# Optimization experiments

Measured on AMD Instinct MI355X. Metric: run time of the kernel, lower is better.

Reference implementation:

```python
import jax, jax.numpy as jnp
import numpy as np
import math

H = 16  # n_heads


def setup_inputs() -> dict:
    key = jax.random.key(0)
    ks = jax.random.split(key, 12)
    B, S, D = 8, 1024, 1024
    inp = {
        "query": jax.random.normal(ks[0], (B, S, D), jnp.float32),
        "key_": jax.random.normal(ks[1], (B, S, D), jnp.float32),
        "value": jax.random.normal(ks[2], (B, S, D), jnp.float32),
        "mask": jnp.ones((B, S, S), jnp.int32),
        "attn_pos": jax.random.normal(ks[3], (1, H, S, S), jnp.float32),
    }
    sc = 1.0 / math.sqrt(D)
    for i, nm in enumerate(["q", "k", "v", "o"]):
        inp[f"w{nm}"] = jax.random.normal(ks[4 + i], (D, D), jnp.float32) * sc
        inp[f"b{nm}"] = jax.random.normal(ks[8 + i], (D,), jnp.float32) * 0.01
    return inp


def reference(query, key_, value, mask, attn_pos, wq, bq, wk, bk, wv, bv, wo, bo):
    B, S, D = query.shape
    dk = D // H

    def proj(x, w, b):  # [B,S,D] -> [B,H,S,dk]
        return (x @ w.T + b).reshape(B, S, H, dk).transpose(0, 2, 1, 3)

    q = proj(query, wq, bq)
    k = proj(key_, wk, bk)
    v = proj(value, wv, bv)

    # attn_pos branch: scale by sqrt(2*d_k), add positional bias
    scores = jnp.einsum("bhqd,bhkd->bhqk", q, k) / math.sqrt(2 * dk) + attn_pos
    scores = jnp.where(mask[:, None] == 0, -1e9, scores)
    p = jax.nn.softmax(scores, axis=-1)  # dropout inactive (eval)
    x = jnp.einsum("bhqk,bhkd->bhqd", p, v)
    x = x.transpose(0, 2, 1, 3).reshape(B, S, D)
    x = x @ wo.T + bo          # linears[-1] applied once...
    return x @ wo.T + bo       # ...and again, faithful to source
```

## Files before the change

kernel.cpp:

```cpp
#include <hip/hip_runtime.h>
#include <hip/hip_bf16.h>

typedef unsigned short u16;
typedef unsigned int u32;
typedef __attribute__((ext_vector_type(8))) short bfrag;
typedef __attribute__((ext_vector_type(4))) float f32x4;

#define DEVINL __device__ __forceinline__

DEVINL u16 f2bf(float f) {
  u32 u = __float_as_uint(f);
  u32 r = (u + 0x7fffu + ((u >> 16) & 1u)) >> 16;
  return (u16)r;
}
DEVINL float bf2f(u16 u) { return __uint_as_float(((u32)u) << 16); }
DEVINL u32 cvtpk(float lo, float hi) {
  u32 r;
  asm("v_cvt_pk_bf16_f32 %0, %1, %2" : "=v"(r) : "v"(lo), "v"(hi));
  return r;
}
DEVINL u16 f2bf_hw(float v) { return (u16)cvtpk(v, v); }
DEVINL float fmax3(float a, float b, float c) { return fmaxf(fmaxf(a, b), c); }

DEVINL void gload_lds16(const void* g, void* l) {
  __builtin_amdgcn_global_load_lds(
      (const __attribute__((address_space(1))) void*)g,
      (__attribute__((address_space(3))) void*)l, 16, 0, 0);
}

DEVINL void storeC(u16* C, size_t idx, float v) { C[idx] = f2bf_hw(v); }
DEVINL void storeC(float* C, size_t idx, float v) { C[idx] = v; }


__global__ void cast_v4(const float* __restrict__ in, u16* __restrict__ out, int n4, float s) {
  const int i = blockIdx.x * 256 + threadIdx.x;
  if (i < n4) {
    const float4 f = ((const float4*)in)[i];
    uint2 r;
    r.x = cvtpk(f.x * s, f.y * s);
    r.y = cvtpk(f.z * s, f.w * s);
    ((uint2*)out)[i] = r;
  }
}

__global__ void pack_mask(const int* __restrict__ mask, u32* __restrict__ bits) {
  const size_t wi = (size_t)blockIdx.x * 256 + threadIdx.x;
  const int* src = mask + wi * 32;
  u32 v = 0;
#pragma unroll
  for (int i = 0; i < 8; ++i) {
    const int4 m4 = ((const int4*)src)[i];
    if (m4.x) v |= 1u << (i * 4 + 0);
    if (m4.y) v |= 1u << (i * 4 + 1);
    if (m4.z) v |= 1u << (i * 4 + 2);
    if (m4.w) v |= 1u << (i * 4 + 3);
  }
  bits[wi] = v;
}

__global__ void transpose_cast(const float* __restrict__ in, u16* __restrict__ out) {
  __shared__ u16 tile[64][65];
  const int t = threadIdx.x;
  const int bx = blockIdx.x, by = blockIdx.y;
#pragma unroll
  for (int p = 0; p < 4; ++p) {
    const int r = (t >> 4) + p * 16;
    const int c = (t & 15) * 4;
    const float4 f = *(const float4*)&in[(size_t)(by * 64 + r) * 1024 + bx * 64 + c];
    tile[c + 0][r] = f2bf(f.x);
    tile[c + 1][r] = f2bf(f.y);
    tile[c + 2][r] = f2bf(f.z);
    tile[c + 3][r] = f2bf(f.w);
  }
  __syncthreads();
#pragma unroll
  for (int p = 0; p < 4; ++p) {
    const int r = (t >> 4) + p * 16;
    const int c = (t & 15) * 4;
    uint2 v;
    v.x = (u32)tile[r][c] | ((u32)tile[r][c + 1] << 16);
    v.y = (u32)tile[r][c + 2] | ((u32)tile[r][c + 3] << 16);
    *(uint2*)&out[(size_t)(bx * 64 + r) * 1024 + by * 64 + c] = v;
  }
}

__global__ void bias2(const float* __restrict__ wo, const float* __restrict__ bo,
                      float* __restrict__ bo2) {
  const int w = threadIdx.x >> 6, lane = threadIdx.x & 63;
  const int row = blockIdx.x * 4 + w;
  const float* src = wo + (size_t)row * 1024;
  float s = 0.f;
#pragma unroll
  for (int i = 0; i < 4; ++i) {
    const float4 f = *(const float4*)&src[lane * 4 + i * 256];
    const float4 g = *(const float4*)&bo[lane * 4 + i * 256];
    s += f.x * g.x + f.y * g.y + f.z * g.z + f.w * g.w;
  }
#pragma unroll
  for (int d = 1; d < 64; d <<= 1) s += __shfl_xor(s, d);
  if (lane == 0) bo2[row] = s + bo[row];
}

__global__ __launch_bounds__(256) void gemm_bt_64(
    const u16* __restrict__ A, const u16* __restrict__ W,
    u16* __restrict__ C, int N, int K) {
  __shared__ u16 sA[64 * 64];
  __shared__ u16 sB[64 * 64];
  const int t = threadIdx.x;
  const int w = t >> 6, lane = t & 63;
  const int lr = lane & 15, lk = (lane >> 4) * 8;
  const int m0 = blockIdx.x * 64, n0 = blockIdx.y * 64;
  f32x4 acc[4] = {};
  for (int k0 = 0; k0 < K; k0 += 64) {
#pragma unroll
    for (int i = 0; i < 2; ++i) {
      const int idx = i * 256 + t;
      const int row = idx >> 3;
      const int col = (idx & 7) * 8;
      gload_lds16(A + (size_t)(m0 + row) * K + k0 + col, &sA[idx * 8]);
      gload_lds16(W + (size_t)(n0 + row) * K + k0 + col, &sB[idx * 8]);
    }
    __syncthreads();
#pragma unroll
    for (int ks = 0; ks < 2; ++ks) {
      const bfrag av = *(const bfrag*)&sA[(w * 16 + lr) * 64 + ks * 32 + lk];
#pragma unroll
      for (int n = 0; n < 4; ++n) {
        const bfrag bv = *(const bfrag*)&sB[(n * 16 + lr) * 64 + ks * 32 + lk];
        acc[n] = __builtin_amdgcn_mfma_f32_16x16x32_bf16(av, bv, acc[n], 0, 0, 0);
      }
    }
    __syncthreads();
  }
  const int orow = (lane >> 4) * 4;
#pragma unroll
  for (int n = 0; n < 4; ++n)
#pragma unroll
    for (int j = 0; j < 4; ++j)
      C[(size_t)(m0 + w * 16 + orow + j) * N + n0 + n * 16 + lr] = f2bf_hw(acc[n][j]);
}


template <typename OutT>
__global__ __launch_bounds__(256) void gemm_bt_a16(
    const u16* __restrict__ A, const u16* __restrict__ W,
    const float* __restrict__ bias, OutT* __restrict__ C,
    int M, int N, int K) {
  __shared__ __align__(16) u16 sA[128 * 64];
  __shared__ __align__(16) u16 sB[128 * 64];
  const int t = threadIdx.x;
  const int w = t >> 6, lane = t & 63;
  const int lr = lane & 15, lg = lane >> 4;
  const int m0 = blockIdx.x * 128, n0 = blockIdx.y * 128;
  const int wr = (w >> 1) * 64, wc = (w & 1) * 64;
  f32x4 acc[4][4] = {};

  for (int k0 = 0; k0 < K; k0 += 64) {
#pragma unroll
    for (int i = 0; i < 4; ++i) {
      const int idx = i * 256 + t;
      const int row = idx >> 3;
      const int col = ((idx & 7) ^ (row & 7)) * 8;
      gload_lds16(A + (size_t)(m0 + row) * K + k0 + col, (char*)sA + idx * 16);
      gload_lds16(W + (size_t)(n0 + row) * K + k0 + col, (char*)sB + idx * 16);
    }
    __syncthreads();
#pragma unroll
    for (int ks = 0; ks < 2; ++ks) {
      bfrag av[4], bv[4];
#pragma unroll
      for (int m = 0; m < 4; ++m) {
        const int row = wr + m * 16 + lr;
        av[m] = *(const bfrag*)((const char*)sA + row * 128 + ((ks * 64 + lg * 16) ^ ((row & 7) << 4)));
      }
#pragma unroll
      for (int n = 0; n < 4; ++n) {
        const int row = wc + n * 16 + lr;
        bv[n] = *(const bfrag*)((const char*)sB + row * 128 + ((ks * 64 + lg * 16) ^ ((row & 7) << 4)));
      }
#pragma unroll
      for (int m = 0; m < 4; ++m)
#pragma unroll
        for (int n = 0; n < 4; ++n)
          acc[m][n] = __builtin_amdgcn_mfma_f32_16x16x32_bf16(av[m], bv[n], acc[m][n], 0, 0, 0);
    }
    __syncthreads();
  }

  float bz[4];
#pragma unroll
  for (int n = 0; n < 4; ++n) bz[n] = bias[n0 + wc + n * 16 + lr];
  const int orow = lg * 4;
#pragma unroll
  for (int m = 0; m < 4; ++m) {
#pragma unroll
    for (int n = 0; n < 4; ++n) {
      const int r = m0 + wr + m * 16 + orow;
      const int c = n0 + wc + n * 16 + lr;
#pragma unroll
      for (int j = 0; j < 4; ++j)
        storeC(C, (size_t)(r + j) * N + c, acc[m][n][j] + bz[n]);
    }
  }
}

template <typename OutT>
__global__ __launch_bounds__(256) void gemm_bt_a32(
    const float* __restrict__ A, const u16* __restrict__ W,
    const float* __restrict__ bias, OutT* __restrict__ C,
    int M, int N, int K, float oscale) {
  __shared__ __align__(16) u16 sA[128 * 64];
  __shared__ __align__(16) u16 sB[128 * 64];
  const int t = threadIdx.x;
  const int w = t >> 6, lane = t & 63;
  const int lr = lane & 15, lg = lane >> 4;
  const int m0 = blockIdx.x * 128, n0 = blockIdx.y * 128;
  const int wr = (w >> 1) * 64, wc = (w & 1) * 64;
  f32x4 acc[4][4] = {};

  for (int k0 = 0; k0 < K; k0 += 64) {
#pragma unroll
    for (int i = 0; i < 4; ++i) {
      const int idx = i * 256 + t;
      const int row = idx >> 3;
      const int cg = idx & 7;
      const float* src = A + (size_t)(m0 + row) * K + k0 + cg * 8;
      const float4 f0 = *(const float4*)src;
      const float4 f1 = *(const float4*)(src + 4);
      uint4 pk;
      pk.x = cvtpk(f0.x, f0.y);
      pk.y = cvtpk(f0.z, f0.w);
      pk.z = cvtpk(f1.x, f1.y);
      pk.w = cvtpk(f1.z, f1.w);
      *(uint4*)((char*)sA + row * 128 + ((cg ^ (row & 7)) * 16)) = pk;
      gload_lds16(W + (size_t)(n0 + row) * K + k0 + ((cg ^ (row & 7)) * 8), (char*)sB + idx * 16);
    }
    __syncthreads();
#pragma unroll
    for (int ks = 0; ks < 2; ++ks) {
      bfrag av[4], bv[4];
#pragma unroll
      for (int m = 0; m < 4; ++m) {
        const int row = wr + m * 16 + lr;
        av[m] = *(const bfrag*)((const char*)sA + row * 128 + ((ks * 64 + lg * 16) ^ ((row & 7) << 4)));
      }
#pragma unroll
      for (int n = 0; n < 4; ++n) {
        const int row = wc + n * 16 + lr;
        bv[n] = *(const bfrag*)((const char*)sB + row * 128 + ((ks * 64 + lg * 16) ^ ((row & 7) << 4)));
      }
#pragma unroll
      for (int m = 0; m < 4; ++m)
#pragma unroll
        for (int n = 0; n < 4; ++n)
          acc[m][n] = __builtin_amdgcn_mfma_f32_16x16x32_bf16(av[m], bv[n], acc[m][n], 0, 0, 0);
    }
    __syncthreads();
  }

  float bz[4];
#pragma unroll
  for (int n = 0; n < 4; ++n) bz[n] = bias[n0 + wc + n * 16 + lr];
  const int orow = lg * 4;
#pragma unroll
  for (int m = 0; m < 4; ++m) {
#pragma unroll
    for (int n = 0; n < 4; ++n) {
      const int r = m0 + wr + m * 16 + orow;
      const int c = n0 + wc + n * 16 + lr;
#pragma unroll
      for (int j = 0; j < 4; ++j)
        storeC(C, (size_t)(r + j) * N + c, (acc[m][n][j] + bz[n]) * oscale);
    }
  }
}

__global__ __launch_bounds__(256) void gemm_bt_a32_vt(
    const float* __restrict__ A, const u16* __restrict__ W,
    const float* __restrict__ bias, u16* __restrict__ Vt,
    int M, int N, int K) {
  __shared__ __align__(16) u16 sA[128 * 64];
  __shared__ __align__(16) u16 sB[128 * 64];
  const int t = threadIdx.x;
  const int w = t >> 6, lane = t & 63;
  const int lr = lane & 15, lg = lane >> 4;
  const int m0 = blockIdx.x * 128, n0 = blockIdx.y * 128;
  const int wr = (w >> 1) * 64, wc = (w & 1) * 64;
  f32x4 acc[4][4] = {};

  for (int k0 = 0; k0 < K; k0 += 64) {
#pragma unroll
    for (int i = 0; i < 4; ++i) {
      const int idx = i * 256 + t;
      const int row = idx >> 3;
      const int cg = idx & 7;
      const float* src = A + (size_t)(m0 + row) * K + k0 + cg * 8;
      const float4 f0 = *(const float4*)src;
      const float4 f1 = *(const float4*)(src + 4);
      uint4 pk;
      pk.x = cvtpk(f0.x, f0.y);
      pk.y = cvtpk(f0.z, f0.w);
      pk.z = cvtpk(f1.x, f1.y);
      pk.w = cvtpk(f1.z, f1.w);
      *(uint4*)((char*)sA + row * 128 + ((cg ^ (row & 7)) * 16)) = pk;
      gload_lds16(W + (size_t)(n0 + row) * K + k0 + ((cg ^ (row & 7)) * 8), (char*)sB + idx * 16);
    }
    __syncthreads();
#pragma unroll
    for (int ks = 0; ks < 2; ++ks) {
      bfrag av[4], bv[4];
#pragma unroll
      for (int m = 0; m < 4; ++m) {
        const int row = wr + m * 16 + lr;
        av[m] = *(const bfrag*)((const char*)sA + row * 128 + ((ks * 64 + lg * 16) ^ ((row & 7) << 4)));
      }
#pragma unroll
      for (int n = 0; n < 4; ++n) {
        const int row = wc + n * 16 + lr;
        bv[n] = *(const bfrag*)((const char*)sB + row * 128 + ((ks * 64 + lg * 16) ^ ((row & 7) << 4)));
      }
#pragma unroll
      for (int m = 0; m < 4; ++m)
#pragma unroll
        for (int n = 0; n < 4; ++n)
          acc[m][n] = __builtin_amdgcn_mfma_f32_16x16x32_bf16(av[m], bv[n], acc[m][n], 0, 0, 0);
    }
    __syncthreads();
  }

  float bz[4];
#pragma unroll
  for (int n = 0; n < 4; ++n) bz[n] = bias[n0 + wc + n * 16 + lr];
  const int orow = lg * 4;
#pragma unroll
  for (int m = 0; m < 4; ++m) {
#pragma unroll
    for (int n = 0; n < 4; ++n) {
      const int r0 = m0 + wr + m * 16 + orow;
      const int c = n0 + wc + n * 16 + lr;
      const int bb = r0 >> 10, s = r0 & 1023;
      const int h = c >> 6, d = c & 63;
      uint2 v;
      v.x = cvtpk(acc[m][n][0] + bz[n], acc[m][n][1] + bz[n]);
      v.y = cvtpk(acc[m][n][2] + bz[n], acc[m][n][3] + bz[n]);
      *(uint2*)&Vt[(((size_t)bb * 16 + h) * 64 + d) * 1024 + s] = v;
    }
  }
}


__global__ __launch_bounds__(512, 4) void attn_fwd(
    const u16* __restrict__ Qm, const u16* __restrict__ Km,
    const u16* __restrict__ Vt, const float* __restrict__ pos,
    const u32* __restrict__ mbits, u16* __restrict__ Om) {
  const int bb = blockIdx.x >> 3;
  const int qt = blockIdx.x & 7;
  const int h = blockIdx.y;
  const int t = threadIdx.x;
  const int w = t >> 6, lane = t & 63;
  const int lr = lane & 15, lg = lane >> 4;
  const float log2e = 1.4426950408889634f;

  __shared__ __align__(16) char smem[49152];

  const int q0 = qt * 128;
  const size_t baseQ = ((size_t)bb * 1024) * 1024 + (size_t)h * 64;
  const size_t baseV = ((size_t)(bb * 16 + h) * 64) * 1024;
  const int qg = q0 + w * 16 + lr;
  const float* posrow = pos + ((size_t)h * 1024 + qg) * 1024;
  const u32* mrow = mbits + ((size_t)bb * 1024 + qg) * 32;

#pragma unroll
  for (int i = 0; i < 2; ++i) {
    const int idx = i * 512 + t;
    const int r = idx >> 3;
    const int w8 = idx & 7;
    gload_lds16(Qm + baseQ + (size_t)(q0 + r) * 1024 + (w8 ^ (r & 7)) * 8, smem + idx * 16);
  }
  {
    const int r = t >> 3;
    const int w8 = t & 7;
    gload_lds16(Km + baseQ + (size_t)r * 1024 + (w8 ^ (r & 7)) * 8, smem + 16384 + t * 16);
    gload_lds16(Vt + baseV + (size_t)r * 1024 + (w8 ^ (r & 7)) * 8, smem + 24576 + t * 16);
  }

  u32 ok = 0xffffffffu;
#pragma unroll
  for (int i = 0; i < 8; ++i) {
    const uint4 m4 = *(const uint4*)&mrow[i * 4];
    ok &= m4.x & m4.y & m4.z & m4.w;
  }
  const bool allone = __all(ok == 0xffffffffu);

  float4 pz[4];
#pragma unroll
  for (int n = 0; n < 4; ++n) pz[n] = *(const float4*)&posrow[n * 16 + lg * 4];

  __syncthreads();

  bfrag qv[2];
#pragma unroll
  for (int ks = 0; ks < 2; ++ks) {
    const int byt = (w * 16 + lr) * 128 + ((ks * 64 + lg * 16) ^ ((lr & 7) << 4));
    qv[ks] = *(const bfrag*)(smem + byt);
  }
  __syncthreads();

  f32x4 o[4] = {};
  float m_q = -3.0e38f, l_q = 0.f;

  for (int kt = 0; kt < 16; ++kt) {
    const int cur = kt & 1;
    const char* sK = smem + (cur ? 0 : 16384);
    const char* sV = smem + (cur ? 8192 : 24576);

    float4 pzn[4];
    if (kt < 15) {
      const int kn = (kt + 1) * 64;
      char* dK = smem + (cur ? 16384 : 0);
      char* dV = smem + (cur ? 24576 : 8192);
      const int r = t >> 3;
      const int w8 = t & 7;
      gload_lds16(Km + baseQ + (size_t)(kn + r) * 1024 + (w8 ^ (r & 7)) * 8, dK + t * 16);
      gload_lds16(Vt + baseV + (size_t)r * 1024 + kn + (w8 ^ (r & 7)) * 8, dV + t * 16);
#pragma unroll
      for (int n = 0; n < 4; ++n) pzn[n] = *(const float4*)&posrow[kn + n * 16 + lg * 4];
    }

    f32x4 s[4] = {};
    __builtin_amdgcn_s_setprio(1);
#pragma unroll
    for (int ks = 0; ks < 2; ++ks) {
#pragma unroll
      for (int n = 0; n < 4; ++n) {
        const int byt = (n * 16 + lr) * 128 + ((ks * 64 + lg * 16) ^ ((lr & 7) << 4));
        const bfrag kf = *(const bfrag*)(sK + byt);
        s[n] = __builtin_amdgcn_mfma_f32_16x16x32_bf16(kf, qv[ks], s[n], 0, 0, 0);
      }
    }
    __builtin_amdgcn_s_setprio(0);

    float pv[16];
#pragma unroll
    for (int n = 0; n < 4; ++n) {
      pv[n * 4 + 0] = fmaf(pz[n].x, log2e, s[n][0]);
      pv[n * 4 + 1] = fmaf(pz[n].y, log2e, s[n][1]);
      pv[n * 4 + 2] = fmaf(pz[n].z, log2e, s[n][2]);
      pv[n * 4 + 3] = fmaf(pz[n].w, log2e, s[n][3]);
    }

    if (!allone) {
      const u32 a0 = mrow[kt * 2], a1 = mrow[kt * 2 + 1];
#pragma unroll
      for (int n = 0; n < 4; ++n)
#pragma unroll
        for (int j = 0; j < 4; ++j) {
          const int kl = n * 16 + lg * 4 + j;
          const u32 mw = (kl & 32) ? a1 : a0;
          if (!((mw >> (kl & 31)) & 1u)) pv[n * 4 + j] = -1.0e9f;
        }
    }

    float tmax = fmax3(pv[0], pv[1], pv[2]);
    tmax = fmax3(tmax, pv[3], pv[4]);
    tmax = fmax3(tmax, pv[5], pv[6]);
    tmax = fmax3(tmax, pv[7], pv[8]);
    tmax = fmax3(tmax, pv[9], pv[10]);
    tmax = fmax3(tmax, pv[11], pv[12]);
    tmax = fmax3(tmax, pv[13], pv[14]);
    tmax = fmaxf(tmax, pv[15]);
    tmax = fmaxf(tmax, __shfl_xor(tmax, 16));
    tmax = fmaxf(tmax, __shfl_xor(tmax, 32));

    if (!__all(tmax <= m_q + 8.0f)) {
      const float mn = fmaxf(m_q, tmax);
      const float sc = __builtin_amdgcn_exp2f(m_q - mn);
      l_q *= sc;
#pragma unroll
      for (int j = 0; j < 4; ++j) {
        const float scj = __shfl(sc, lg * 4 + j);
#pragma unroll
        for (int n = 0; n < 4; ++n) o[n][j] *= scj;
      }
      m_q = mn;
    }
    float rs = 0.f;
#pragma unroll
    for (int i2 = 0; i2 < 16; ++i2) {
      pv[i2] = __builtin_amdgcn_exp2f(pv[i2] - m_q);
      rs += pv[i2];
    }
    rs += __shfl_xor(rs, 16);
    rs += __shfl_xor(rs, 32);
    l_q += rs;

    char* pbuf = smem + 32768 + w * 2048;
#pragma unroll
    for (int n = 0; n < 4; ++n) {
      uint2 pk;
      pk.x = cvtpk(pv[n * 4 + 0], pv[n * 4 + 1]);
      pk.y = cvtpk(pv[n * 4 + 2], pv[n * 4 + 3]);
      const int byt = lr * 128 + ((n * 32 + lg * 8) ^ ((lr & 7) << 4));
      *(uint2*)(pbuf + byt) = pk;
    }
    __builtin_amdgcn_s_setprio(1);
#pragma unroll
    for (int ks = 0; ks < 2; ++ks) {
      const int pbyt = lr * 128 + ((ks * 64 + lg * 16) ^ ((lr & 7) << 4));
      const bfrag pf = *(const bfrag*)(pbuf + pbyt);
#pragma unroll
      for (int n = 0; n < 4; ++n) {
        const int vb = (n * 16 + lr) * 128 + ((ks * 64 + lg * 16) ^ ((lr & 7) << 4));
        const bfrag vf = *(const bfrag*)(sV + vb);
        o[n] = __builtin_amdgcn_mfma_f32_16x16x32_bf16(pf, vf, o[n], 0, 0, 0);
      }
    }
    __builtin_amdgcn_s_setprio(0);

    __syncthreads();

    if (kt < 15) {
#pragma unroll
      for (int n = 0; n < 4; ++n) pz[n] = pzn[n];
    }
  }

#pragma unroll
  for (int j = 0; j < 4; ++j) {
    const float lj = __shfl(l_q, lg * 4 + j);
    const float inv = 1.f / lj;
    const int qr = q0 + w * 16 + lg * 4 + j;
#pragma unroll
    for (int n = 0; n < 4; ++n)
      Om[baseQ + (size_t)qr * 1024 + n * 16 + lr] = f2bf_hw(o[n][j] * inv);
  }
}


extern "C" void kernel_launch(void* const* d_in, const int* in_sizes, int n_in,
                              void* d_out, int out_size, void* d_ws, size_t ws_size,
                              hipStream_t stream) {
  const float* query = (const float*)d_in[0];
  const float* key_  = (const float*)d_in[1];
  const float* value = (const float*)d_in[2];
  const int*   mask  = (const int*)d_in[3];
  const float* pos   = (const float*)d_in[4];
  const float* wq = (const float*)d_in[5];
  const float* bq = (const float*)d_in[6];
  const float* wk = (const float*)d_in[7];
  const float* bk = (const float*)d_in[8];
  const float* wv = (const float*)d_in[9];
  const float* bv = (const float*)d_in[10];
  const float* wo = (const float*)d_in[11];
  const float* bo = (const float*)d_in[12];

  char* ws = (char*)d_ws;
  const size_t MB = 1024 * 1024;
  u16* wqb  = (u16*)(ws + 0 * MB);
  u16* wkb  = (u16*)(ws + 2 * MB);
  u16* wvb  = (u16*)(ws + 4 * MB);
  u16* wob  = (u16*)(ws + 6 * MB);
  u16* Qb   = (u16*)(ws + 40 * MB);
  u16* Kb   = (u16*)(ws + 56 * MB);
  u16* Vtb  = (u16*)(ws + 72 * MB);
  u16* Xa   = (u16*)(ws + 88 * MB);
  u32* mb   = (u32*)(ws + 104 * MB);
  u16* wotb = (u16*)(ws + 105 * MB);
  u16* W2b  = (u16*)(ws + 107 * MB);
  float* bo2 = (float*)(ws + 109 * MB);

  const float log2e = 1.4426950408889634f;
  const float qs = 0.0883883476483184f * log2e;

  cast_v4<<<1024, 256, 0, stream>>>(wq, wqb, 262144, 1.0f);
  cast_v4<<<1024, 256, 0, stream>>>(wk, wkb, 262144, 1.0f);
  cast_v4<<<1024, 256, 0, stream>>>(wv, wvb, 262144, 1.0f);
  cast_v4<<<1024, 256, 0, stream>>>(wo, wob, 262144, 1.0f);
  pack_mask<<<1024, 256, 0, stream>>>(mask, mb);
  transpose_cast<<<dim3(16, 16), 256, 0, stream>>>(wo, wotb);
  bias2<<<256, 256, 0, stream>>>(wo, bo, bo2);

  gemm_bt_64<<<dim3(16, 16), 256, 0, stream>>>(wob, wotb, W2b, 1024, 1024);

  const dim3 gg(64, 8);
  gemm_bt_a32<u16><<<gg, 256, 0, stream>>>(query, wqb, bq, Qb, 8192, 1024, 1024, qs);
  gemm_bt_a32<u16><<<gg, 256, 0, stream>>>(key_,  wkb, bk, Kb, 8192, 1024, 1024, 1.0f);
  gemm_bt_a32_vt<<<gg, 256, 0, stream>>>(value, wvb, bv, Vtb, 8192, 1024, 1024);

  attn_fwd<<<dim3(64, 16), 512, 0, stream>>>(Qb, Kb, Vtb, pos, mb, Xa);

  gemm_bt_a16<float><<<gg, 256, 0, stream>>>(Xa, W2b, bo2, (float*)d_out, 8192, 1024, 1024);
}
```

Before: 260.8 us.

## Batch QKV projections into one launch, double-buffer output GEMM, remap block grids

Merges the four weight-cast kernels into one launch and the three Q/K/V projection GEMMs into a single 1536-block kernel. The QKV kernel issues its fp32 A loads for a K-step before the barrier so that load latency overlaps the previous step's compute. The output GEMM gets double-buffered LDS with prefetch of the next K tile, using explicit waitcnt and barriers. Block IDs in the GEMMs and the attention kernel are remapped to group tiles that share data (L2 locality). These changes target launch overhead and memory latency, at the cost of more LDS use in the output GEMM and possibly lower occupancy.

```diff
diff --git a/kernel.cpp b/kernel.cpp
--- a/kernel.cpp
+++ b/kernel.cpp
@@ -31,16 +31,29 @@
 DEVINL void storeC(u16* C, size_t idx, float v) { C[idx] = f2bf_hw(v); }
 DEVINL void storeC(float* C, size_t idx, float v) { C[idx] = v; }
 
-
-__global__ void cast_v4(const float* __restrict__ in, u16* __restrict__ out, int n4, float s) {
-  const int i = blockIdx.x * 256 + threadIdx.x;
-  if (i < n4) {
-    const float4 f = ((const float4*)in)[i];
-    uint2 r;
-    r.x = cvtpk(f.x * s, f.y * s);
-    r.y = cvtpk(f.z * s, f.w * s);
-    ((uint2*)out)[i] = r;
-  }
+#define SBAR0 __builtin_amdgcn_sched_barrier(0)
+
+DEVINL void gemm_decode(int gid, int& m0, int& n0) {
+  const int m = ((gid >> 6) << 3) | (gid & 7);
+  const int n = (gid >> 3) & 7;
+  m0 = m * 128;
+  n0 = n * 128;
+}
+
+
+__global__ void cast_w4(const float* __restrict__ w0, const float* __restrict__ w1,
+                        const float* __restrict__ w2, const float* __restrict__ w3,
+                        u16* __restrict__ o0, u16* __restrict__ o1,
+                        u16* __restrict__ o2, u16* __restrict__ o3) {
+  const int which = blockIdx.x >> 10;
+  const int i = (blockIdx.x & 1023) * 256 + threadIdx.x;
+  const float* in = which == 0 ? w0 : which == 1 ? w1 : which == 2 ? w2 : w3;
+  u16* out = which == 0 ? o0 : which == 1 ? o1 : which == 2 ? o2 : o3;
+  const float4 f = ((const float4*)in)[i];
+  uint2 r;
+  r.x = cvtpk(f.x, f.y);
+  r.y = cvtpk(f.z, f.w);
+  ((uint2*)out)[i] = r;
 }
 
 __global__ void pack_mask(const int* __restrict__ mask, u32* __restrict__ bits) {
@@ -141,42 +154,167 @@
 }
 
 
+__global__ __launch_bounds__(256) void gemm_qkv(
+    const float* __restrict__ Aq, const float* __restrict__ Ak, const float* __restrict__ Av,
+    const u16* __restrict__ Wq, const u16* __restrict__ Wk, const u16* __restrict__ Wv,
+    const float* __restrict__ Bq, const float* __restrict__ Bk, const float* __restrict__ Bv,
+    u16* __restrict__ Qb, u16* __restrict__ Kb, u16* __restrict__ Vt, float qs) {
+  __shared__ __align__(16) u16 sA[128 * 64];
+  __shared__ __align__(16) u16 sB[128 * 64];
+  const int gid = blockIdx.x;
+  const int which = gid >> 9;
+  int m0, n0;
+  gemm_decode(gid & 511, m0, n0);
+  const float* A = which == 0 ? Aq : which == 1 ? Ak : Av;
+  const u16* W = which == 0 ? Wq : which == 1 ? Wk : Wv;
+  const float* bias = which == 0 ? Bq : which == 1 ? Bk : Bv;
+  const int t = threadIdx.x;
+  const int w = t >> 6, lane = t & 63;
+  const int lr = lane & 15, lg = lane >> 4;
+  const int wr = (w >> 1) * 64, wc = (w & 1) * 64;
+  f32x4 acc[4][4] = {};
+
+  for (int kt = 0; kt < 16; ++kt) {
+    const int k0 = kt * 64;
+    f32x4 fa[4][2];
+#pragma unroll
+    for (int i = 0; i < 4; ++i) {
+      const int idx = i * 256 + t;
+      const int row = idx >> 3;
+      const int cg = idx & 7;
+      const float* src = A + (size_t)(m0 + row) * 1024 + k0 + cg * 8;
+      fa[i][0] = *(const f32x4*)src;
+      fa[i][1] = *(const f32x4*)(src + 4);
+    }
+    if (kt) __syncthreads();
+#pragma unroll
+    for (int i = 0; i < 4; ++i) {
+      const int idx = i * 256 + t;
+      const int row = idx >> 3;
+      const int cg = idx & 7;
+      uint4 pk;
+      pk.x = cvtpk(fa[i][0][0], fa[i][0][1]);
+      pk.y = cvtpk(fa[i][0][2], fa[i][0][3]);
+      pk.z = cvtpk(fa[i][1][0], fa[i][1][1]);
+      pk.w = cvtpk(fa[i][1][2], fa[i][1][3]);
+      *(uint4*)((char*)sA + row * 128 + ((cg ^ (row & 7)) * 16)) = pk;
+      gload_lds16(W + (size_t)(n0 + row) * 1024 + k0 + ((cg ^ (row & 7)) * 8),
+                  (char*)sB + idx * 16);
+    }
+    __syncthreads();
+#pragma unroll
+    for (int ks = 0; ks < 2; ++ks) {
+      bfrag av[4], bv[4];
+#pragma unroll
+      for (int m = 0; m < 4; ++m) {
+        const int row = wr + m * 16 + lr;
+        av[m] = *(const bfrag*)((const char*)sA + row * 128 + ((ks * 64 + lg * 16) ^ ((row & 7) << 4)));
+      }
+#pragma unroll
+      for (int n = 0; n < 4; ++n) {
+        const int row = wc + n * 16 + lr;
+        bv[n] = *(const bfrag*)((const char*)sB + row * 128 + ((ks * 64 + lg * 16) ^ ((row & 7) << 4)));
+      }
+#pragma unroll
+      for (int m = 0; m < 4; ++m)
+#pragma unroll
+        for (int n = 0; n < 4; ++n)
+          acc[m][n] = __builtin_amdgcn_mfma_f32_16x16x32_bf16(av[m], bv[n], acc[m][n], 0, 0, 0);
+    }
+  }
+
+  float bz[4];
+#pragma unroll
+  for (int n = 0; n < 4; ++n) bz[n] = bias[n0 + wc + n * 16 + lr];
+  const int orow = lg * 4;
+  if (which == 2) {
+#pragma unroll
+    for (int m = 0; m < 4; ++m) {
+#pragma unroll
+      for (int n = 0; n < 4; ++n) {
+        const int r0 = m0 + wr + m * 16 + orow;
+        const int c = n0 + wc + n * 16 + lr;
+        const int bb = r0 >> 10, s = r0 & 1023;
+        const int h = c >> 6, d = c & 63;
+        uint2 v;
+        v.x = cvtpk(acc[m][n][0] + bz[n], acc[m][n][1] + bz[n]);
+        v.y = cvtpk(acc[m][n][2] + bz[n], acc[m][n][3] + bz[n]);
+        *(uint2*)&Vt[(((size_t)bb * 16 + h) * 64 + d) * 1024 + s] = v;
+      }
+    }
+  } else {
+    u16* C = which == 0 ? Qb : Kb;
+    const float osc = which == 0 ? qs : 1.0f;
+#pragma unroll
+    for (int m = 0; m < 4; ++m) {
+#pragma unroll
+      for (int n = 0; n < 4; ++n) {
+        const int r = m0 + wr + m * 16 + orow;
+        const int c = n0 + wc + n * 16 + lr;
+#pragma unroll
+        for (int j = 0; j < 4; ++j)
+          C[(size_t)(r + j) * 1024 + c] = f2bf_hw((acc[m][n][j] + bz[n]) * osc);
+      }
+    }
+  }
+}
+
+
 template <typename OutT>
 __global__ __launch_bounds__(256) void gemm_bt_a16(
     const u16* __restrict__ A, const u16* __restrict__ W,
     const float* __restrict__ bias, OutT* __restrict__ C,
     int M, int N, int K) {
-  __shared__ __align__(16) u16 sA[128 * 64];
-  __shared__ __align__(16) u16 sB[128 * 64];
+  __shared__ __align__(16) u16 sA[2][128 * 64];
+  __shared__ __align__(16) u16 sB[2][128 * 64];
   const int t = threadIdx.x;
   const int w = t >> 6, lane = t & 63;
   const int lr = lane & 15, lg = lane >> 4;
-  const int m0 = blockIdx.x * 128, n0 = blockIdx.y * 128;
+  int m0, n0;
+  gemm_decode(blockIdx.x, m0, n0);
   const int wr = (w >> 1) * 64, wc = (w & 1) * 64;
   f32x4 acc[4][4] = {};
-
-  for (int k0 = 0; k0 < K; k0 += 64) {
-#pragma unroll
-    for (int i = 0; i < 4; ++i) {
-      const int idx = i * 256 + t;
-      const int row = idx >> 3;
-      const int col = ((idx & 7) ^ (row & 7)) * 8;
-      gload_lds16(A + (size_t)(m0 + row) * K + k0 + col, (char*)sA + idx * 16);
-      gload_lds16(W + (size_t)(n0 + row) * K + k0 + col, (char*)sB + idx * 16);
-    }
-    __syncthreads();
+  const int nk = K >> 6;
+
+#pragma unroll
+  for (int i = 0; i < 4; ++i) {
+    const int idx = i * 256 + t;
+    const int row = idx >> 3;
+    const int col = ((idx & 7) ^ (row & 7)) * 8;
+    gload_lds16(A + (size_t)(m0 + row) * K + col, (char*)sA[0] + idx * 16);
+    gload_lds16(W + (size_t)(n0 + row) * K + col, (char*)sB[0] + idx * 16);
+  }
+  SBAR0; asm volatile("s_waitcnt vmcnt(0)" ::: "memory"); SBAR0;
+  __builtin_amdgcn_s_barrier(); SBAR0;
+
+#pragma unroll 2
+  for (int kt = 0; kt < nk; ++kt) {
+    const int cur = kt & 1;
+    if (kt < nk - 1) {
+      const int k0 = (kt + 1) * 64;
+#pragma unroll
+      for (int i = 0; i < 4; ++i) {
+        const int idx = i * 256 + t;
+        const int row = idx >> 3;
+        const int col = ((idx & 7) ^ (row & 7)) * 8;
+        gload_lds16(A + (size_t)(m0 + row) * K + k0 + col, (char*)sA[cur ^ 1] + idx * 16);
+        gload_lds16(W + (size_t)(n0 + row) * K + k0 + col, (char*)sB[cur ^ 1] + idx * 16);
+      }
+    }
+    const char* pA = (const char*)sA[cur];
+    const char* pB = (const char*)sB[cur];
 #pragma unroll
     for (int ks = 0; ks < 2; ++ks) {
       bfrag av[4], bv[4];
 #pragma unroll
       for (int m = 0; m < 4; ++m) {
         const int row = wr + m * 16 + lr;
-        av[m] = *(const bfrag*)((const char*)sA + row * 128 + ((ks * 64 + lg * 16) ^ ((row & 7) << 4)));
+        av[m] = *(const bfrag*)(pA + row * 128 + ((ks * 64 + lg * 16) ^ ((row & 7) << 4)));
       }
 #pragma unroll
       for (int n = 0; n < 4; ++n) {
         const int row = wc + n * 16 + lr;
-        bv[n] = *(const bfrag*)((const char*)sB + row * 128 + ((ks * 64 + lg * 16) ^ ((row & 7) << 4)));
+        bv[n] = *(const bfrag*)(pB + row * 128 + ((ks * 64 + lg * 16) ^ ((row & 7) << 4)));
       }
 #pragma unroll
       for (int m = 0; m < 4; ++m)
@@ -184,7 +322,10 @@
         for (int n = 0; n < 4; ++n)
           acc[m][n] = __builtin_amdgcn_mfma_f32_16x16x32_bf16(av[m], bv[n], acc[m][n], 0, 0, 0);
     }
-    __syncthreads();
+    if (kt < nk - 1) {
+      SBAR0; asm volatile("s_waitcnt vmcnt(0)" ::: "memory"); SBAR0;
+      __builtin_amdgcn_s_barrier(); SBAR0;
+    }
   }
 
   float bz[4];
@@ -200,150 +341,6 @@
 #pragma unroll
       for (int j = 0; j < 4; ++j)
         storeC(C, (size_t)(r + j) * N + c, acc[m][n][j] + bz[n]);
-    }
-  }
-}
-
-template <typename OutT>
-__global__ __launch_bounds__(256) void gemm_bt_a32(
-    const float* __restrict__ A, const u16* __restrict__ W,
-    const float* __restrict__ bias, OutT* __restrict__ C,
-    int M, int N, int K, float oscale) {
-  __shared__ __align__(16) u16 sA[128 * 64];
-  __shared__ __align__(16) u16 sB[128 * 64];
-  const int t = threadIdx.x;
-  const int w = t >> 6, lane = t & 63;
-  const int lr = lane & 15, lg = lane >> 4;
-  const int m0 = blockIdx.x * 128, n0 = blockIdx.y * 128;
-  const int wr = (w >> 1) * 64, wc = (w & 1) * 64;
-  f32x4 acc[4][4] = {};
-
-  for (int k0 = 0; k0 < K; k0 += 64) {
-#pragma unroll
-    for (int i = 0; i < 4; ++i) {
-      const int idx = i * 256 + t;
-      const int row = idx >> 3;
-      const int cg = idx & 7;
-      const float* src = A + (size_t)(m0 + row) * K + k0 + cg * 8;
-      const float4 f0 = *(const float4*)src;
-      const float4 f1 = *(const float4*)(src + 4);
-      uint4 pk;
-      pk.x = cvtpk(f0.x, f0.y);
-      pk.y = cvtpk(f0.z, f0.w);
-      pk.z = cvtpk(f1.x, f1.y);
-      pk.w = cvtpk(f1.z, f1.w);
-      *(uint4*)((char*)sA + row * 128 + ((cg ^ (row & 7)) * 16)) = pk;
-      gload_lds16(W + (size_t)(n0 + row) * K + k0 + ((cg ^ (row & 7)) * 8), (char*)sB + idx * 16);
-    }
-    __syncthreads();
-#pragma unroll
-    for (int ks = 0; ks < 2; ++ks) {
-      bfrag av[4], bv[4];
-#pragma unroll
-      for (int m = 0; m < 4; ++m) {
-        const int row = wr + m * 16 + lr;
-        av[m] = *(const bfrag*)((const char*)sA + row * 128 + ((ks * 64 + lg * 16) ^ ((row & 7) << 4)));
-      }
-#pragma unroll
-      for (int n = 0; n < 4; ++n) {
-        const int row = wc + n * 16 + lr;
-        bv[n] = *(const bfrag*)((const char*)sB + row * 128 + ((ks * 64 + lg * 16) ^ ((row & 7) << 4)));
-      }
-#pragma unroll
-      for (int m = 0; m < 4; ++m)
-#pragma unroll
-        for (int n = 0; n < 4; ++n)
-          acc[m][n] = __builtin_amdgcn_mfma_f32_16x16x32_bf16(av[m], bv[n], acc[m][n], 0, 0, 0);
-    }
-    __syncthreads();
-  }
-
-  float bz[4];
-#pragma unroll
-  for (int n = 0; n < 4; ++n) bz[n] = bias[n0 + wc + n * 16 + lr];
-  const int orow = lg * 4;
-#pragma unroll
-  for (int m = 0; m < 4; ++m) {
-#pragma unroll
-    for (int n = 0; n < 4; ++n) {
-      const int r = m0 + wr + m * 16 + orow;
-      const int c = n0 + wc + n * 16 + lr;
-#pragma unroll
-      for (int j = 0; j < 4; ++j)
-        storeC(C, (size_t)(r + j) * N + c, (acc[m][n][j] + bz[n]) * oscale);
-    }
-  }
-}
-
-__global__ __launch_bounds__(256) void gemm_bt_a32_vt(
-    const float* __restrict__ A, const u16* __restrict__ W,
-    const float* __restrict__ bias, u16* __restrict__ Vt,
-    int M, int N, int K) {
-  __shared__ __align__(16) u16 sA[128 * 64];
-  __shared__ __align__(16) u16 sB[128 * 64];
-  const int t = threadIdx.x;
-  const int w = t >> 6, lane = t & 63;
-  const int lr = lane & 15, lg = lane >> 4;
-  const int m0 = blockIdx.x * 128, n0 = blockIdx.y * 128;
-  const int wr = (w >> 1) * 64, wc = (w & 1) * 64;
-  f32x4 acc[4][4] = {};
-
-  for (int k0 = 0; k0 < K; k0 += 64) {
-#pragma unroll
-    for (int i = 0; i < 4; ++i) {
-      const int idx = i * 256 + t;
-      const int row = idx >> 3;
-      const int cg = idx & 7;
-      const float* src = A + (size_t)(m0 + row) * K + k0 + cg * 8;
-      const float4 f0 = *(const float4*)src;
-      const float4 f1 = *(const float4*)(src + 4);
-      uint4 pk;
-      pk.x = cvtpk(f0.x, f0.y);
-      pk.y = cvtpk(f0.z, f0.w);
-      pk.z = cvtpk(f1.x, f1.y);
-      pk.w = cvtpk(f1.z, f1.w);
-      *(uint4*)((char*)sA + row * 128 + ((cg ^ (row & 7)) * 16)) = pk;
-      gload_lds16(W + (size_t)(n0 + row) * K + k0 + ((cg ^ (row & 7)) * 8), (char*)sB + idx * 16);
-    }
-    __syncthreads();
-#pragma unroll
-    for (int ks = 0; ks < 2; ++ks) {
-      bfrag av[4], bv[4];
-#pragma unroll
-      for (int m = 0; m < 4; ++m) {
-        const int row = wr + m * 16 + lr;
-        av[m] = *(const bfrag*)((const char*)sA + row * 128 + ((ks * 64 + lg * 16) ^ ((row & 7) << 4)));
-      }
-#pragma unroll
-      for (int n = 0; n < 4; ++n) {
-        const int row = wc + n * 16 + lr;
-        bv[n] = *(const bfrag*)((const char*)sB + row * 128 + ((ks * 64 + lg * 16) ^ ((row & 7) << 4)));
-      }
-#pragma unroll
-      for (int m = 0; m < 4; ++m)
-#pragma unroll
-        for (int n = 0; n < 4; ++n)
-          acc[m][n] = __builtin_amdgcn_mfma_f32_16x16x32_bf16(av[m], bv[n], acc[m][n], 0, 0, 0);
-    }
-    __syncthreads();
-  }
-
-  float bz[4];
-#pragma unroll
-  for (int n = 0; n < 4; ++n) bz[n] = bias[n0 + wc + n * 16 + lr];
-  const int orow = lg * 4;
-#pragma unroll
-  for (int m = 0; m < 4; ++m) {
-#pragma unroll
-    for (int n = 0; n < 4; ++n) {
-      const int r0 = m0 + wr + m * 16 + orow;
-      const int c = n0 + wc + n * 16 + lr;
-      const int bb = r0 >> 10, s = r0 & 1023;
-      const int h = c >> 6, d = c & 63;
-      uint2 v;
-      v.x = cvtpk(acc[m][n][0] + bz[n], acc[m][n][1] + bz[n]);
-      v.y = cvtpk(acc[m][n][2] + bz[n], acc[m][n][3] + bz[n]);
-      *(uint2*)&Vt[(((size_t)bb * 16 + h) * 64 + d) * 1024 + s] = v;
     }
   }
 }
@@ -353,9 +350,11 @@
     const u16* __restrict__ Qm, const u16* __restrict__ Km,
     const u16* __restrict__ Vt, const float* __restrict__ pos,
     const u32* __restrict__ mbits, u16* __restrict__ Om) {
-  const int bb = blockIdx.x >> 3;
-  const int qt = blockIdx.x & 7;
-  const int h = blockIdx.y;
+  const int gid = blockIdx.x;
+  const int h = (gid & 7) + 8 * (gid >> 9);
+  const int inner = (gid >> 3) & 63;
+  const int bb = inner & 7;
+  const int qt = inner >> 3;
   const int t = threadIdx.x;
   const int w = t >> 6, lane = t & 63;
   const int lr = lane & 15, lg = lane >> 4;
@@ -572,22 +571,17 @@
   const float log2e = 1.4426950408889634f;
   const float qs = 0.0883883476483184f * log2e;
 
-  cast_v4<<<1024, 256, 0, stream>>>(wq, wqb, 262144, 1.0f);
-  cast_v4<<<1024, 256, 0, stream>>>(wk, wkb, 262144, 1.0f);
-  cast_v4<<<1024, 256, 0, stream>>>(wv, wvb, 262144, 1.0f);
-  cast_v4<<<1024, 256, 0, stream>>>(wo, wob, 262144, 1.0f);
+  cast_w4<<<4096, 256, 0, stream>>>(wq, wk, wv, wo, wqb, wkb, wvb, wob);
   pack_mask<<<1024, 256, 0, stream>>>(mask, mb);
   transpose_cast<<<dim3(16, 16), 256, 0, stream>>>(wo, wotb);
   bias2<<<256, 256, 0, stream>>>(wo, bo, bo2);
 
   gemm_bt_64<<<dim3(16, 16), 256, 0, stream>>>(wob, wotb, W2b, 1024, 1024);
 
-  const dim3 gg(64, 8);
-  gemm_bt_a32<u16><<<gg, 256, 0, stream>>>(query, wqb, bq, Qb, 8192, 1024, 1024, qs);
-  gemm_bt_a32<u16><<<gg, 256, 0, stream>>>(key_,  wkb, bk, Kb, 8192, 1024, 1024, 1.0f);
-  gemm_bt_a32_vt<<<gg, 256, 0, stream>>>(value, wvb, bv, Vtb, 8192, 1024, 1024);
-
-  attn_fwd<<<dim3(64, 16), 512, 0, stream>>>(Qb, Kb, Vtb, pos, mb, Xa);
-
-  gemm_bt_a16<float><<<gg, 256, 0, stream>>>(Xa, W2b, bo2, (float*)d_out, 8192, 1024, 1024);
-}
+  gemm_qkv<<<1536, 256, 0, stream>>>(query, key_, value, wqb, wkb, wvb,
+                                     bq, bk, bv, Qb, Kb, Vtb, qs);
+
+  attn_fwd<<<1024, 512, 0, stream>>>(Qb, Kb, Vtb, pos, mb, Xa);
+
+  gemm_bt_a16<float><<<512, 256, 0, stream>>>(Xa, W2b, bo2, (float*)d_out, 8192, 1024, 1024);
+}
```

Result: faster. 229.0 us (median of 3 runs) (-12.2%).
